# Kernel tuning notes

Hardware: AMD Instinct MI355X
Metric: run time of the kernel (lower is better)

Reference implementation:

```python
import jax, jax.numpy as jnp
import numpy as np

NUM_CLASSES = 80
GRID = 13
A = 9                      # 3 scales x 3 anchors, flattened
P = GRID * GRID * A        # 1521 priors
OBJ_SCALE, NOOBJ_SCALE, CLS_SCALE, BOX_SCALE = 1.0, 100.0, 1.0, 5.0
ANCHORS_NP = np.array([[10,13],[16,30],[33,23],[30,61],[62,45],[59,119],[116,90],[156,198],[373,326]], dtype=np.float32)


def setup_inputs() -> dict:
    key = jax.random.key(0)
    k1, k2, k3, k4, k5 = jax.random.split(key, 5)
    B, T = 512, 50
    predictions = jax.random.normal(k1, (B, P, 5 + NUM_CLASSES), dtype=jnp.float32)
    xy = jax.random.uniform(k2, (B, T, 2), minval=0.02, maxval=0.98)
    wh = jax.random.uniform(k3, (B, T, 2), minval=0.01, maxval=0.30)
    conf = (jax.random.uniform(k4, (B, T, 1)) < 0.6).astype(jnp.float32)
    cls = jax.random.randint(k5, (B, T, 1), 0, NUM_CLASSES).astype(jnp.float32)
    targets = jnp.concatenate([xy, wh, conf, cls], axis=-1)  # [B,T,6]
    anchors = jnp.asarray(ANCHORS_NP)                        # [9,2]
    return {"predictions": predictions, "targets": targets, "anchors": anchors}


def _safe_log(x):
    # torch BCELoss clamps log terms at -100
    return jnp.maximum(jnp.log(x), -100.0)


def _per_image(pred, tgt, anchors):
    # pred: [P, 5+C], tgt: [T, 6], anchors: [A, 2]
    valid = tgt[:, 4] > 0
    has = jnp.any(valid)
    # wh-only IoU: target wh scaled by 1000 (pixel scale) vs anchor wh
    tw_px = tgt[:, 2] * 1000.0
    th_px = tgt[:, 3] * 1000.0
    aw = anchors[:, 0][:, None]  # [A,1]
    ah = anchors[:, 1][:, None]
    inter = jnp.minimum(aw, tw_px[None, :]) * jnp.minimum(ah, th_px[None, :])  # [A,T]
    union = aw * ah + tw_px * th_px - inter
    iou = inter / (union + 1e-16)
    best_a = jnp.argmax(iou, axis=0)  # [T]
    gx = jnp.floor(tgt[:, 0] * GRID).astype(jnp.int32)
    gy = jnp.floor(tgt[:, 1] * GRID).astype(jnp.int32)
    prior = gy * (GRID * A) + gx * A + best_a
    prior = jnp.where(valid, prior, P)  # invalid targets scatter out-of-range -> dropped

    obj = jnp.zeros((P,), jnp.float32).at[prior].set(1.0, mode='drop')
    txv = tgt[:, 0] * GRID - gx.astype(jnp.float32)
    tyv = tgt[:, 1] * GRID - gy.astype(jnp.float32)
    aw_b = anchors[best_a, 0]
    ah_b = anchors[best_a, 1]
    twv = jnp.log(tgt[:, 2] * GRID / aw_b + 1e-16)
    thv = jnp.log(tgt[:, 3] * GRID / ah_b + 1e-16)
    tx = jnp.zeros((P,), jnp.float32).at[prior].set(txv, mode='drop')
    ty = jnp.zeros((P,), jnp.float32).at[prior].set(tyv, mode='drop')
    tw = jnp.zeros((P,), jnp.float32).at[prior].set(twv, mode='drop')
    th = jnp.zeros((P,), jnp.float32).at[prior].set(thv, mode='drop')
    cls_idx = tgt[:, 5].astype(jnp.int32)
    tcls = jnp.zeros((P, NUM_CLASSES), jnp.float32).at[prior, cls_idx].set(1.0, mode='drop')

    conf_p = jax.nn.sigmoid(pred[:, 4])
    logp = _safe_log(conf_p)
    log1mp = _safe_log(1.0 - conf_p)

    box = BOX_SCALE * jnp.sum(obj * ((pred[:, 0] - tx) ** 2 + (pred[:, 1] - ty) ** 2
                                     + (pred[:, 2] - tw) ** 2 + (pred[:, 3] - th) ** 2))
    objl = -OBJ_SCALE * jnp.sum(obj * logp)
    # empty-image branch: BCE(conf, ones).sum() = -sum(log p); otherwise BCE over noobj priors vs 0
    noobjl = jnp.where(has,
                       -NOOBJ_SCALE * jnp.sum((1.0 - obj) * log1mp),
                       -NOOBJ_SCALE * jnp.sum(logp))
    pcls = jax.nn.sigmoid(pred[:, 5:])
    bce_cls = -(tcls * _safe_log(pcls) + (1.0 - tcls) * _safe_log(1.0 - pcls))
    clsl = CLS_SCALE * jnp.sum(obj[:, None] * bce_cls)
    return box, objl, noobjl, clsl


def reference(predictions, targets, anchors):
    box, objl, noobjl, clsl = jax.vmap(lambda p, t: _per_image(p, t, anchors))(predictions, targets)
    B = predictions.shape[0]
    box_loss = jnp.sum(box) / B
    obj_loss = jnp.sum(objl) / B
    noobj_loss = jnp.sum(noobjl) / B
    cls_loss = jnp.sum(clsl) / B
    total = box_loss + obj_loss + noobj_loss + cls_loss
    return (total, box_loss, obj_loss, noobj_loss, cls_loss)
```

## Files before the change

### kernel.cpp

```cpp
#include <hip/hip_runtime.h>
#include <cmath>

#define B_N 512
#define T_N 50
#define GRIDN 13
#define A_N 9
#define P_N 1521
#define ROW 85
#define NCLS 80
#define FPI (P_N * ROW)
#define NTHR 1024

struct Entry {
    int prior;
    float tx, ty, tw, th;
    unsigned int cls[3];
};

__global__ void __launch_bounds__(NTHR)
main_kernel(const float* __restrict__ pred,
            const float* __restrict__ tgt,
            const float* __restrict__ anchors,
            float* __restrict__ part)
{
    __shared__ Entry ents[T_N];
    __shared__ int   s_cnt;
    __shared__ float red[16][5];

    const int tid  = threadIdx.x;
    const int lane = tid & 63;
    const int b    = blockIdx.x;

    const float* tb = tgt + (size_t)b * T_N * 6;
    float confv = (lane < T_N) ? tb[lane * 6 + 4] : 0.0f;
    const bool hasv = (__ballot(confv > 0.0f) != 0ull);

    const float* slab = pred + (size_t)b * FPI;
    const int a0 = (4 - (b & 3)) & 3;
    const int NQ = (FPI - a0) >> 2;
    const float4* qp = (const float4*)(slab + a0);
    float s_main = 0.0f;
    for (int q = tid; q < NQ; q += NTHR) {
        float4 v = qp[q];
        int f0 = a0 + (q << 2);
        int c0 = f0 % 85;
        if ((unsigned)(c0 - 1) <= 3u) {
            int k = 4 - c0;
            float x = (k == 0) ? v.x : (k == 1) ? v.y : (k == 2) ? v.z : v.w;
            float s = 1.0f / (1.0f + __expf(-x));
            s_main += hasv ? fmaxf(__logf(1.0f - s), -100.0f)
                           : fmaxf(__logf(s),        -100.0f);
        }
    }

    if (tid < 64) {
        int   prior = -1;
        float txv = 0.f, tyv = 0.f, twv = 0.f, thv = 0.f;
        int   cls = 0;
        if (lane < T_N) {
            const float* t = tb + lane * 6;
            float x = t[0], y = t[1], w = t[2], h = t[3], conf = t[4];
            if (conf > 0.0f) {
                float tw_px = w * 1000.0f, th_px = h * 1000.0f;
                int best = 0; float bestv = -1.0f;
                #pragma unroll
                for (int a = 0; a < A_N; ++a) {
                    float aw = anchors[2*a], ah = anchors[2*a+1];
                    float inter = fminf(aw, tw_px) * fminf(ah, th_px);
                    float uni   = aw*ah + tw_px*th_px - inter;
                    float iou   = inter / (uni + 1e-16f);
                    if (iou > bestv) { bestv = iou; best = a; }
                }
                int gx = (int)floorf(x * (float)GRIDN);
                int gy = (int)floorf(y * (float)GRIDN);
                prior = gy * (GRIDN * A_N) + gx * A_N + best;
                txv = x * (float)GRIDN - (float)gx;
                tyv = y * (float)GRIDN - (float)gy;
                float aw = anchors[2*best], ah = anchors[2*best+1];
                twv = logf(w * (float)GRIDN / aw + 1e-16f);
                thv = logf(h * (float)GRIDN / ah + 1e-16f);
                cls = (int)t[5];
            }
        }
        bool valid = (prior >= 0);
        unsigned int m0 = 0, m1 = 0, m2 = 0;
        bool laterdup = false;
        #pragma unroll
        for (int j = 0; j < T_N; ++j) {
            int pj = __shfl(prior, j, 64);
            int cj = __shfl(cls,   j, 64);
            if (valid && pj == prior) {
                if (j > lane) laterdup = true;
                if (cj < 32)      m0 |= 1u << cj;
                else if (cj < 64) m1 |= 1u << (cj - 32);
                else              m2 |= 1u << (cj - 64);
            }
        }
        bool winner = valid && !laterdup;
        unsigned long long mask = __ballot(winner);
        if (winner) {
            int idx = __popcll(mask & ((1ull << lane) - 1ull));
            Entry* e = &ents[idx];
            e->prior = prior;
            e->tx = txv; e->ty = tyv; e->tw = twv; e->th = thv;
            e->cls[0] = m0; e->cls[1] = m1; e->cls[2] = m2;
        }
        if (lane == 0) s_cnt = __popcll(mask);
    }
    __syncthreads();

    const int cnt = s_cnt;

    float cls_s = 0.0f, box_s = 0.0f, objlp = 0.0f, objl1 = 0.0f;
    {
        const int gid = tid >> 7;
        const int lt  = tid & 127;
        for (int e = gid; e < cnt; e += 8) {
            Entry en = ents[e];
            const float* row = slab + (size_t)en.prior * ROW;
            if (lt < NCLS) {
                float x  = row[5 + lt];
                float s  = 1.0f / (1.0f + __expf(-x));
                float lp = fmaxf(__logf(s),        -100.0f);
                float l1 = fmaxf(__logf(1.0f - s), -100.0f);
                float tc = ((en.cls[lt >> 5] >> (lt & 31)) & 1u) ? 1.0f : 0.0f;
                cls_s += -(tc * lp + (1.0f - tc) * l1);
            } else if (lt == NCLS) {
                float x = row[4];
                float s = 1.0f / (1.0f + __expf(-x));
                objlp += fmaxf(__logf(s),        -100.0f);
                objl1 += fmaxf(__logf(1.0f - s), -100.0f);
            } else if (lt == NCLS + 1) {
                float d0 = row[0] - en.tx;
                float d1 = row[1] - en.ty;
                float d2 = row[2] - en.tw;
                float d3 = row[3] - en.th;
                box_s += d0*d0 + d1*d1 + d2*d2 + d3*d3;
            }
        }
    }

    float v0 = s_main, v1 = objl1, v2 = objlp, v3 = box_s, v4 = cls_s;
    #pragma unroll
    for (int o = 32; o > 0; o >>= 1) {
        v0 += __shfl_down(v0, o, 64);
        v1 += __shfl_down(v1, o, 64);
        v2 += __shfl_down(v2, o, 64);
        v3 += __shfl_down(v3, o, 64);
        v4 += __shfl_down(v4, o, 64);
    }
    const int w = tid >> 6;
    if (lane == 0) {
        red[w][0] = v0; red[w][1] = v1; red[w][2] = v2;
        red[w][3] = v3; red[w][4] = v4;
    }
    __syncthreads();
    if (tid < 5) {
        float s = 0.0f;
        #pragma unroll
        for (int ww = 0; ww < 16; ++ww) s += red[ww][tid];
        part[(size_t)b * 5 + tid] = s;
    }
}

__global__ void __launch_bounds__(256)
finalize_kernel(const float* __restrict__ part, float* __restrict__ out)
{
    __shared__ float red[4][4];
    const int tid  = threadIdx.x;
    const int lane = tid & 63;

    float a_box = 0, a_obj = 0, a_noobj = 0, a_cls = 0;
    for (int b = tid; b < B_N; b += 256) {
        const float* p = part + (size_t)b * 5;
        float S  = p[0];
        float L1 = p[1];
        float LP = p[2];
        float BX = p[3];
        float CL = p[4];
        a_box   += 5.0f * BX;
        a_obj   += -LP;
        a_noobj += -100.0f * (S - L1);
        a_cls   += CL;
    }
    #pragma unroll
    for (int o = 32; o > 0; o >>= 1) {
        a_box   += __shfl_down(a_box,   o, 64);
        a_obj   += __shfl_down(a_obj,   o, 64);
        a_noobj += __shfl_down(a_noobj, o, 64);
        a_cls   += __shfl_down(a_cls,   o, 64);
    }
    const int w = tid >> 6;
    if (lane == 0) { red[w][0] = a_box; red[w][1] = a_obj; red[w][2] = a_noobj; red[w][3] = a_cls; }
    __syncthreads();
    if (tid == 0) {
        const float invB = 1.0f / (float)B_N;
        float box   = (red[0][0] + red[1][0] + red[2][0] + red[3][0]) * invB;
        float obj   = (red[0][1] + red[1][1] + red[2][1] + red[3][1]) * invB;
        float noobj = (red[0][2] + red[1][2] + red[2][2] + red[3][2]) * invB;
        float cls   = (red[0][3] + red[1][3] + red[2][3] + red[3][3]) * invB;
        out[0] = box + obj + noobj + cls;
        out[1] = box;
        out[2] = obj;
        out[3] = noobj;
        out[4] = cls;
    }
}

extern "C" void kernel_launch(void* const* d_in, const int* in_sizes, int n_in,
                              void* d_out, int out_size, void* d_ws, size_t ws_size,
                              hipStream_t stream)
{
    const float* pred    = (const float*)d_in[0];
    const float* tgt     = (const float*)d_in[1];
    const float* anchors = (const float*)d_in[2];
    float* out  = (float*)d_out;
    float* part = (float*)d_ws;

    main_kernel<<<dim3(B_N), dim3(NTHR), 0, stream>>>(pred, tgt, anchors, part);
    finalize_kernel<<<dim3(1), dim3(256), 0, stream>>>(part, out);
}
```

Baseline: 54.72 us.

## Process two images per block with dense and sparse conf-column readers

Each block now handles two images. For one image, 768 threads stream the whole slab with vector loads, as before. For the other, 256 threads gather only the conf column with strided scalar loads, which skips most of that image's bytes. The BCE uses a softplus form with a sign flip instead of sigmoid plus log, and the modulo is replaced by an incremental counter. The sparse gather touches a fraction of the cache lines, but the hardware still fetches whole lines, so the bandwidth saving may be partial, and the grid halves to 256 blocks.

```diff
diff --git a/kernel.cpp b/kernel.cpp
--- a/kernel.cpp
+++ b/kernel.cpp
@@ -10,6 +10,10 @@
 #define NCLS 80
 #define FPI (P_N * ROW)
 #define NTHR 1024
+#define G_HALF 256
+#define DTHR 768
+
+typedef float f32x4 __attribute__((ext_vector_type(4)));
 
 struct Entry {
     int prior;
@@ -17,119 +21,156 @@
     unsigned int cls[3];
 };
 
+__device__ __forceinline__ float bce_neg(float z) {
+    float sp = fmaxf(z, 0.0f) + __logf(1.0f + __expf(-fabsf(z)));
+    return fmaxf(-sp, -100.0f);
+}
+
+__device__ __forceinline__ void build_entries(const float* __restrict__ tb,
+                                              const float* __restrict__ anchors,
+                                              int lane, Entry* ents, int* s_cnt)
+{
+    int   prior = -1;
+    float txv = 0.f, tyv = 0.f, twv = 0.f, thv = 0.f;
+    int   cls = 0;
+    if (lane < T_N) {
+        const float* t = tb + lane * 6;
+        float x = t[0], y = t[1], w = t[2], h = t[3], conf = t[4];
+        if (conf > 0.0f) {
+            float tw_px = w * 1000.0f, th_px = h * 1000.0f;
+            int best = 0; float bestv = -1.0f;
+            #pragma unroll
+            for (int a = 0; a < A_N; ++a) {
+                float aw = anchors[2*a], ah = anchors[2*a+1];
+                float inter = fminf(aw, tw_px) * fminf(ah, th_px);
+                float uni   = aw*ah + tw_px*th_px - inter;
+                float iou   = inter / (uni + 1e-16f);
+                if (iou > bestv) { bestv = iou; best = a; }
+            }
+            int gx = (int)floorf(x * (float)GRIDN);
+            int gy = (int)floorf(y * (float)GRIDN);
+            prior = gy * (GRIDN * A_N) + gx * A_N + best;
+            txv = x * (float)GRIDN - (float)gx;
+            tyv = y * (float)GRIDN - (float)gy;
+            float aw = anchors[2*best], ah = anchors[2*best+1];
+            twv = logf(w * (float)GRIDN / aw + 1e-16f);
+            thv = logf(h * (float)GRIDN / ah + 1e-16f);
+            cls = (int)t[5];
+        }
+    }
+    bool valid = (prior >= 0);
+    unsigned int m0 = 0, m1 = 0, m2 = 0;
+    bool laterdup = false;
+    #pragma unroll
+    for (int j = 0; j < T_N; ++j) {
+        int pj = __shfl(prior, j, 64);
+        int cj = __shfl(cls,   j, 64);
+        if (valid && pj == prior) {
+            if (j > lane) laterdup = true;
+            if (cj < 32)      m0 |= 1u << cj;
+            else if (cj < 64) m1 |= 1u << (cj - 32);
+            else              m2 |= 1u << (cj - 64);
+        }
+    }
+    bool winner = valid && !laterdup;
+    unsigned long long mask = __ballot(winner);
+    if (winner) {
+        int idx = __popcll(mask & ((1ull << lane) - 1ull));
+        Entry* e = &ents[idx];
+        e->prior = prior;
+        e->tx = txv; e->ty = tyv; e->tw = twv; e->th = thv;
+        e->cls[0] = m0; e->cls[1] = m1; e->cls[2] = m2;
+    }
+    if (lane == 0) *s_cnt = __popcll(mask);
+}
+
 __global__ void __launch_bounds__(NTHR)
 main_kernel(const float* __restrict__ pred,
             const float* __restrict__ tgt,
             const float* __restrict__ anchors,
             float* __restrict__ part)
 {
-    __shared__ Entry ents[T_N];
-    __shared__ int   s_cnt;
-    __shared__ float red[16][5];
+    __shared__ Entry ents_d[T_N], ents_s[T_N];
+    __shared__ int   cnt_d, cnt_s;
+    __shared__ float red[16][10];
 
     const int tid  = threadIdx.x;
     const int lane = tid & 63;
-    const int b    = blockIdx.x;
-
-    const float* tb = tgt + (size_t)b * T_N * 6;
-    float confv = (lane < T_N) ? tb[lane * 6 + 4] : 0.0f;
-    const bool hasv = (__ballot(confv > 0.0f) != 0ull);
-
-    const float* slab = pred + (size_t)b * FPI;
-    const int a0 = (4 - (b & 3)) & 3;
-    const int NQ = (FPI - a0) >> 2;
-    const float4* qp = (const float4*)(slab + a0);
-    float s_main = 0.0f;
-    for (int q = tid; q < NQ; q += NTHR) {
-        float4 v = qp[q];
-        int f0 = a0 + (q << 2);
-        int c0 = f0 % 85;
-        if ((unsigned)(c0 - 1) <= 3u) {
-            int k = 4 - c0;
-            float x = (k == 0) ? v.x : (k == 1) ? v.y : (k == 2) ? v.z : v.w;
-            float s = 1.0f / (1.0f + __expf(-x));
-            s_main += hasv ? fmaxf(__logf(1.0f - s), -100.0f)
-                           : fmaxf(__logf(s),        -100.0f);
-        }
-    }
-
-    if (tid < 64) {
-        int   prior = -1;
-        float txv = 0.f, tyv = 0.f, twv = 0.f, thv = 0.f;
-        int   cls = 0;
-        if (lane < T_N) {
-            const float* t = tb + lane * 6;
-            float x = t[0], y = t[1], w = t[2], h = t[3], conf = t[4];
-            if (conf > 0.0f) {
-                float tw_px = w * 1000.0f, th_px = h * 1000.0f;
-                int best = 0; float bestv = -1.0f;
-                #pragma unroll
-                for (int a = 0; a < A_N; ++a) {
-                    float aw = anchors[2*a], ah = anchors[2*a+1];
-                    float inter = fminf(aw, tw_px) * fminf(ah, th_px);
-                    float uni   = aw*ah + tw_px*th_px - inter;
-                    float iou   = inter / (uni + 1e-16f);
-                    if (iou > bestv) { bestv = iou; best = a; }
-                }
-                int gx = (int)floorf(x * (float)GRIDN);
-                int gy = (int)floorf(y * (float)GRIDN);
-                prior = gy * (GRIDN * A_N) + gx * A_N + best;
-                txv = x * (float)GRIDN - (float)gx;
-                tyv = y * (float)GRIDN - (float)gy;
-                float aw = anchors[2*best], ah = anchors[2*best+1];
-                twv = logf(w * (float)GRIDN / aw + 1e-16f);
-                thv = logf(h * (float)GRIDN / ah + 1e-16f);
-                cls = (int)t[5];
-            }
-        }
-        bool valid = (prior >= 0);
-        unsigned int m0 = 0, m1 = 0, m2 = 0;
-        bool laterdup = false;
-        #pragma unroll
-        for (int j = 0; j < T_N; ++j) {
-            int pj = __shfl(prior, j, 64);
-            int cj = __shfl(cls,   j, 64);
-            if (valid && pj == prior) {
-                if (j > lane) laterdup = true;
-                if (cj < 32)      m0 |= 1u << cj;
-                else if (cj < 64) m1 |= 1u << (cj - 32);
-                else              m2 |= 1u << (cj - 64);
-            }
-        }
-        bool winner = valid && !laterdup;
-        unsigned long long mask = __ballot(winner);
-        if (winner) {
-            int idx = __popcll(mask & ((1ull << lane) - 1ull));
-            Entry* e = &ents[idx];
-            e->prior = prior;
-            e->tx = txv; e->ty = tyv; e->tw = twv; e->th = thv;
-            e->cls[0] = m0; e->cls[1] = m1; e->cls[2] = m2;
-        }
-        if (lane == 0) s_cnt = __popcll(mask);
-    }
+    const int wv   = tid >> 6;
+    const int bd   = blockIdx.x;
+    const int bs   = blockIdx.x + G_HALF;
+
+    const float* tbd   = tgt + (size_t)bd * T_N * 6;
+    const float* tbs   = tgt + (size_t)bs * T_N * 6;
+    const float* slabd = pred + (size_t)bd * FPI;
+    const float* slabs = pred + (size_t)bs * FPI;
+
+    float confd = (lane < T_N) ? tbd[lane * 6 + 4] : 0.0f;
+    const float sgnd = (__ballot(confd > 0.0f) != 0ull) ? 1.0f : -1.0f;
+    float confs = (lane < T_N) ? tbs[lane * 6 + 4] : 0.0f;
+    const float sgns = (__ballot(confs > 0.0f) != 0ull) ? 1.0f : -1.0f;
+
+    float acc[10];
+    #pragma unroll
+    for (int i = 0; i < 10; ++i) acc[i] = 0.0f;
+
+    if (tid < DTHR) {
+        const int a0 = (4 - (bd & 3)) & 3;
+        const int NQ = (FPI - a0) >> 2;
+        const f32x4* qp = (const f32x4*)(slabd + a0);
+        int c0 = (a0 + (tid << 2)) % 85;
+        float s = 0.0f;
+        for (int q = tid; q < NQ; q += DTHR) {
+            f32x4 v = qp[q];
+            if ((unsigned)(c0 - 1) <= 3u)
+                s += bce_neg(sgnd * v[4 - c0]);
+            c0 += 12; if (c0 >= 85) c0 -= 85;
+        }
+        acc[0] = s;
+    } else {
+        const int stid = tid - DTHR;
+        float xs[6];
+        #pragma unroll
+        for (int k = 0; k < 6; ++k) {
+            int p = stid + (k << 8);
+            xs[k] = (p < P_N) ? slabs[85 * p + 4] : 0.0f;
+        }
+        float s = 0.0f;
+        #pragma unroll
+        for (int k = 0; k < 6; ++k) {
+            int p = stid + (k << 8);
+            if (p < P_N) s += bce_neg(sgns * xs[k]);
+        }
+        acc[5] = s;
+    }
+
+    if (wv == 0)  build_entries(tbd, anchors, lane, ents_d, &cnt_d);
+    if (wv == 12) build_entries(tbs, anchors, lane, ents_s, &cnt_s);
     __syncthreads();
 
-    const int cnt = s_cnt;
-
-    float cls_s = 0.0f, box_s = 0.0f, objlp = 0.0f, objl1 = 0.0f;
     {
-        const int gid = tid >> 7;
-        const int lt  = tid & 127;
-        for (int e = gid; e < cnt; e += 8) {
+        const bool   lo   = (tid < 512);
+        const float* slab = lo ? slabd : slabs;
+        const Entry* ents = lo ? ents_d : ents_s;
+        const int    cnt  = lo ? cnt_d  : cnt_s;
+        const int    gid  = (tid >> 7) & 3;
+        const int    lt   = tid & 127;
+        float cls_s = 0.f, box_s = 0.f, objlp = 0.f, objl1 = 0.f;
+        for (int e = gid; e < cnt; e += 4) {
             Entry en = ents[e];
             const float* row = slab + (size_t)en.prior * ROW;
             if (lt < NCLS) {
                 float x  = row[5 + lt];
-                float s  = 1.0f / (1.0f + __expf(-x));
-                float lp = fmaxf(__logf(s),        -100.0f);
-                float l1 = fmaxf(__logf(1.0f - s), -100.0f);
+                float sg = 1.0f / (1.0f + __expf(-x));
+                float lp = fmaxf(__logf(sg),        -100.0f);
+                float l1 = fmaxf(__logf(1.0f - sg), -100.0f);
                 float tc = ((en.cls[lt >> 5] >> (lt & 31)) & 1u) ? 1.0f : 0.0f;
                 cls_s += -(tc * lp + (1.0f - tc) * l1);
             } else if (lt == NCLS) {
-                float x = row[4];
-                float s = 1.0f / (1.0f + __expf(-x));
-                objlp += fmaxf(__logf(s),        -100.0f);
-                objl1 += fmaxf(__logf(1.0f - s), -100.0f);
+                float x  = row[4];
+                float sg = 1.0f / (1.0f + __expf(-x));
+                objlp += fmaxf(__logf(sg),        -100.0f);
+                objl1 += fmaxf(__logf(1.0f - sg), -100.0f);
             } else if (lt == NCLS + 1) {
                 float d0 = row[0] - en.tx;
                 float d1 = row[1] - en.ty;
@@ -138,28 +179,29 @@
                 box_s += d0*d0 + d1*d1 + d2*d2 + d3*d3;
             }
         }
-    }
-
-    float v0 = s_main, v1 = objl1, v2 = objlp, v3 = box_s, v4 = cls_s;
+        const int off = lo ? 1 : 6;
+        acc[off + 0] = objl1;
+        acc[off + 1] = objlp;
+        acc[off + 2] = box_s;
+        acc[off + 3] = cls_s;
+    }
+
     #pragma unroll
     for (int o = 32; o > 0; o >>= 1) {
-        v0 += __shfl_down(v0, o, 64);
-        v1 += __shfl_down(v1, o, 64);
-        v2 += __shfl_down(v2, o, 64);
-        v3 += __shfl_down(v3, o, 64);
-        v4 += __shfl_down(v4, o, 64);
-    }
-    const int w = tid >> 6;
+        #pragma unroll
+        for (int i = 0; i < 10; ++i) acc[i] += __shfl_down(acc[i], o, 64);
+    }
     if (lane == 0) {
-        red[w][0] = v0; red[w][1] = v1; red[w][2] = v2;
-        red[w][3] = v3; red[w][4] = v4;
+        #pragma unroll
+        for (int i = 0; i < 10; ++i) red[wv][i] = acc[i];
     }
     __syncthreads();
-    if (tid < 5) {
+    if (tid < 10) {
         float s = 0.0f;
         #pragma unroll
-        for (int ww = 0; ww < 16; ++ww) s += red[ww][tid];
-        part[(size_t)b * 5 + tid] = s;
+        for (int w = 0; w < 16; ++w) s += red[w][tid];
+        if (tid < 5) part[(size_t)bd * 5 + tid]       = s;
+        else         part[(size_t)bs * 5 + (tid - 5)] = s;
     }
 }
 
@@ -217,6 +259,6 @@
     float* out  = (float*)d_out;
     float* part = (float*)d_ws;
 
-    main_kernel<<<dim3(B_N), dim3(NTHR), 0, stream>>>(pred, tgt, anchors, part);
+    main_kernel<<<dim3(G_HALF), dim3(NTHR), 0, stream>>>(pred, tgt, anchors, part);
     finalize_kernel<<<dim3(1), dim3(256), 0, stream>>>(part, out);
 }
```

After: 63.76 us. +16.5%, slower.
